# Optimization experiments

Measured on AMD Instinct MI355X. Metric: run time of the kernel, lower is better.

The kernel has to match this reference:

```python
import jax, jax.numpy as jnp
import numpy as np

B, S, HID = 1, 2048, 2048
NH, NKV, D = 16, 8, 128
N_REP = NH // NKV
EPS = 1e-6
ROPE_THETA = 10000.0
N_VISION = 512  # first 512 tokens are vision, rest text


def rms_norm(x, w):
    # RMSNorm over last dim (head_dim), Qwen3 style per-head norm
    var = jnp.mean(x * x, axis=-1, keepdims=True)
    return x * jax.lax.rsqrt(var + EPS) * w


def rotate_half(x):
    half = x.shape[-1] // 2
    return jnp.concatenate([-x[..., half:], x[..., :half]], axis=-1)


def setup_inputs() -> dict:
    key = jax.random.key(0)
    ks = jax.random.split(key, 8)
    std = 0.02
    hidden_states = jax.random.normal(ks[0], (B, S, HID), jnp.float32)
    wq = jax.random.normal(ks[1], (HID, NH * D), jnp.float32) * std
    wk = jax.random.normal(ks[2], (HID, NKV * D), jnp.float32) * std
    wv = jax.random.normal(ks[3], (HID, NKV * D), jnp.float32) * std
    wo = jax.random.normal(ks[4], (NH * D, HID), jnp.float32) * std
    q_norm_w = jnp.ones((D,), jnp.float32)
    k_norm_w = jnp.ones((D,), jnp.float32)
    # RoPE tables: [1, S, D]
    pos = jnp.arange(S, dtype=jnp.float32)
    inv_freq = 1.0 / (ROPE_THETA ** (jnp.arange(0, D, 2, dtype=jnp.float32) / D))
    freqs = pos[:, None] * inv_freq[None, :]            # [S, D/2]
    emb = jnp.concatenate([freqs, freqs], axis=-1)       # [S, D]
    cos = jnp.cos(emb)[None]
    sin = jnp.sin(emb)[None]
    # additive causal mask [1,1,S,S]: 0 on/below diagonal, -1e9 above
    causal = jnp.tril(jnp.ones((S, S), jnp.bool_))
    attention_mask = jnp.where(causal, 0.0, -1e9).astype(jnp.float32)[None, None]
    # vision/text token masks [B, S]
    idx = jnp.arange(S)
    vision_mask = (idx < N_VISION)[None].astype(jnp.bool_)
    text_mask = jnp.logical_not(vision_mask)
    return {
        'hidden_states': hidden_states, 'wq': wq, 'wk': wk, 'wv': wv, 'wo': wo,
        'q_norm_w': q_norm_w, 'k_norm_w': k_norm_w, 'cos': cos, 'sin': sin,
        'attention_mask': attention_mask, 'vision_mask': vision_mask, 'text_mask': text_mask,
    }


def reference(hidden_states, wq, wk, wv, wo, q_norm_w, k_norm_w, cos, sin,
              attention_mask, vision_mask, text_mask):
    b, s, _ = hidden_states.shape
    # projections + per-head RMSNorm (q/k) -> [B, H, S, D]
    q = rms_norm((hidden_states @ wq).reshape(b, s, NH, D), q_norm_w).transpose(0, 2, 1, 3)
    k = rms_norm((hidden_states @ wk).reshape(b, s, NKV, D), k_norm_w).transpose(0, 2, 1, 3)
    v = (hidden_states @ wv).reshape(b, s, NKV, D).transpose(0, 2, 1, 3)
    # RoPE
    c = cos[:, None]  # [B,1,S,D]
    sn = sin[:, None]
    q = q * c + rotate_half(q) * sn
    k = k * c + rotate_half(k) * sn
    # GQA repeat_kv
    k = jnp.repeat(k, N_REP, axis=1)
    v = jnp.repeat(v, N_REP, axis=1)
    scaling = D ** -0.5
    scores = jnp.einsum('bhqd,bhkd->bhqk', q, k) * scaling + attention_mask
    attn = jax.nn.softmax(scores.astype(jnp.float32), axis=-1)  # [B,H,S,S]
    attn_out = jnp.einsum('bhqk,bhkd->bhqd', attn, v)
    attn_out = attn_out.transpose(0, 2, 1, 3).reshape(b, s, NH * D)
    out = attn_out @ wo  # [B,S,HID]
    # cross head scores (original runs this under no_grad on an identical eager pass)
    attn_ng = jax.lax.stop_gradient(attn)
    vm = vision_mask.astype(jnp.float32)  # [B,S]
    tm = text_mask.astype(jnp.float32)
    nv = vm.sum(-1)  # [B]
    nt = tm.sum(-1)
    v2t = jnp.einsum('bhqk,bq,bk->bh', attn_ng, vm, tm) / jnp.maximum(nv, 1.0)[:, None]
    t2v = jnp.einsum('bhqk,bq,bk->bh', attn_ng, tm, vm) / jnp.maximum(nt, 1.0)[:, None]
    valid = ((nv > 0) & (nt > 0)).astype(jnp.float32)  # [B]
    cross_scores = jnp.sum((v2t + t2v) * valid[:, None], axis=0) / jnp.maximum(valid.sum(), 1.0)
    return out, cross_scores
```

## Files before the change

### kernel.cpp

```cpp
#include <hip/hip_runtime.h>
#include <hip/hip_bf16.h>
#include <stdint.h>

typedef unsigned short u16;
typedef unsigned int u32;
typedef short s16x8 __attribute__((ext_vector_type(8)));
typedef float f32x4 __attribute__((ext_vector_type(4)));

#define S_LEN 2048
#define SCALE 0.088388347648318447f
#define NEG_BIG (-1.0e9f)

__device__ __forceinline__ u16 f2bf(float f) {
  unsigned u = __builtin_bit_cast(unsigned, f);
  u += 0x7fffu + ((u >> 16) & 1u);
  return (u16)(u >> 16);
}
__device__ __forceinline__ float bf2f(u16 h) {
  unsigned u = ((unsigned)h) << 16;
  return __builtin_bit_cast(float, u);
}
__device__ __forceinline__ void gload16(const void* g, void* l) {
  __builtin_amdgcn_global_load_lds((const __attribute__((address_space(1))) void*)g,
                                   (__attribute__((address_space(3))) void*)l, 16, 0, 0);
}

__device__ __forceinline__ void do_transpose(const float* __restrict__ in, u16* __restrict__ out,
                                             int R, int C, int rel, int tilesx) {
  __shared__ float tile[32][33];
  int bx = (rel % tilesx) * 32, by = (rel / tilesx) * 32;
  int tx = threadIdx.x & 31, ty = threadIdx.x >> 5;
#pragma unroll
  for (int i = 0; i < 4; i++)
    tile[ty + i * 8][tx] = in[(size_t)(by + ty + i * 8) * C + bx + tx];
  __syncthreads();
#pragma unroll
  for (int i = 0; i < 4; i++)
    out[(size_t)(bx + ty + i * 8) * R + by + tx] = f2bf(tile[tx][ty + i * 8]);
}

__global__ __launch_bounds__(256) void prep_k(const float* __restrict__ hs, u16* __restrict__ hsb,
                                              const float* __restrict__ wq, const float* __restrict__ wk,
                                              const float* __restrict__ wv, const float* __restrict__ wo,
                                              u16* __restrict__ wqkvT, u16* __restrict__ woT) {
  int bid = blockIdx.x;
  if (bid < 4096) {
    int i = bid * 256 + threadIdx.x;
    float4 v = ((const float4*)hs)[i];
    ushort4 o;
    o.x = f2bf(v.x); o.y = f2bf(v.y); o.z = f2bf(v.z); o.w = f2bf(v.w);
    ((ushort4*)hsb)[i] = o;
  } else if (bid < 8192) {
    do_transpose(wq, wqkvT, 2048, 2048, bid - 4096, 64);
  } else if (bid < 10240) {
    do_transpose(wk, wqkvT + (size_t)2048 * 2048, 2048, 1024, bid - 8192, 32);
  } else if (bid < 12288) {
    do_transpose(wv, wqkvT + (size_t)3072 * 2048, 2048, 1024, bid - 10240, 32);
  } else {
    do_transpose(wo, woT, 2048, 2048, bid - 12288, 64);
  }
}

template <int F32OUT>
__global__ __launch_bounds__(256, 2) void gemm_bt_k(const u16* __restrict__ A, const u16* __restrict__ BT,
                                                    void* __restrict__ Cout, int N, int K) {
  __shared__ u16 lA[2][128 * 64];
  __shared__ u16 lB[2][128 * 64];
  int tid = threadIdx.x;
  int w = tid >> 6, l = tid & 63, r = l & 15, g = l >> 4;
  int tn = blockIdx.x, tm = blockIdx.y;
  int wm = w >> 1, wn = w & 1;
  f32x4 zf = {0.f, 0.f, 0.f, 0.f};
  f32x4 acc[4][4];
#pragma unroll
  for (int mi = 0; mi < 4; mi++)
#pragma unroll
    for (int ni = 0; ni < 4; ni++) acc[mi][ni] = zf;
  int nkt = K >> 6;

  int srow = tid >> 3;
  int soff = (tid & 7) * 16;
  auto stage = [&](int bi, int kt) {
#pragma unroll
    for (int i = 0; i < 4; i++) {
      int row = i * 32 + srow;
      int sb = soff ^ ((row & 7) << 4);
      int L = (i * 256 + tid) * 16;
      gload16(A + (size_t)(tm * 128 + row) * K + kt * 64 + (sb >> 1), (char*)(&lA[bi][0]) + L);
      gload16(BT + (size_t)(tn * 128 + row) * K + kt * 64 + (sb >> 1), (char*)(&lB[bi][0]) + L);
    }
  };
  auto compute = [&](int bi) {
    const char* AB = (const char*)&lA[bi][0];
    const char* BB = (const char*)&lB[bi][0];
#pragma unroll
    for (int kk = 0; kk < 2; kk++) {
      s16x8 af[4], bfr[4];
#pragma unroll
      for (int mi = 0; mi < 4; mi++) {
        int row = wm * 64 + mi * 16 + r;
        af[mi] = *(const s16x8*)(AB + ((row * 128 + kk * 64 + g * 16) ^ ((r & 7) << 4)));
      }
#pragma unroll
      for (int ni = 0; ni < 4; ni++) {
        int row = wn * 64 + ni * 16 + r;
        bfr[ni] = *(const s16x8*)(BB + ((row * 128 + kk * 64 + g * 16) ^ ((r & 7) << 4)));
      }
#pragma unroll
      for (int mi = 0; mi < 4; mi++)
#pragma unroll
        for (int ni = 0; ni < 4; ni++)
          acc[mi][ni] = __builtin_amdgcn_mfma_f32_16x16x32_bf16(af[mi], bfr[ni], acc[mi][ni], 0, 0, 0);
    }
  };

  stage(0, 0);
  __syncthreads();
  int cur = 0;
  for (int kt = 0; kt + 1 < nkt; ++kt) {
    stage(cur ^ 1, kt + 1);
    compute(cur);
    __syncthreads();
    cur ^= 1;
  }
  compute(cur);

#pragma unroll
  for (int mi = 0; mi < 4; mi++) {
#pragma unroll
    for (int ni = 0; ni < 4; ni++) {
#pragma unroll
      for (int j = 0; j < 4; j++) {
        int row = tm * 128 + wm * 64 + mi * 16 + g * 4 + j;
        int col = tn * 128 + wn * 64 + ni * 16 + r;
        if (F32OUT)
          ((float*)Cout)[(size_t)row * N + col] = acc[mi][ni][j];
        else
          ((u16*)Cout)[(size_t)row * N + col] = f2bf(acc[mi][ni][j]);
      }
    }
  }
}

__global__ __launch_bounds__(256) void post_k(const u16* __restrict__ qkv, const float* __restrict__ qw,
                                              const float* __restrict__ kw, const float* __restrict__ cosT,
                                              const float* __restrict__ sinT, u16* __restrict__ Qb,
                                              u16* __restrict__ Kb, u16* __restrict__ Vt,
                                              float* __restrict__ cross) {
  int bid = blockIdx.x;
  int tid = threadIdx.x;
  if (bid == 0 && tid < 16) cross[tid] = 0.f;
  if (bid < 16384) {
    int gw = bid * 4 + (tid >> 6);
    int l = tid & 63;
    int s = gw >> 5, slot = gw & 31;
    if (slot >= 24) return;
    const float* nw;
    const u16* src;
    u16* dst;
    if (slot < 16) {
      src = qkv + (size_t)s * 4096 + slot * 128;
      nw = qw;
      dst = Qb + ((size_t)slot * S_LEN + s) * 128;
    } else {
      int hk = slot - 16;
      src = qkv + (size_t)s * 4096 + 2048 + hk * 128;
      nw = kw;
      dst = Kb + ((size_t)hk * S_LEN + s) * 128;
    }
    ushort2 xv = ((const ushort2*)src)[l];
    float x0 = bf2f(xv.x), x1 = bf2f(xv.y);
    float ss = x0 * x0 + x1 * x1;
#pragma unroll
    for (int off = 1; off < 64; off <<= 1) ss += __shfl_xor(ss, off);
    float inv = rsqrtf(ss * (1.0f / 128.0f) + 1e-6f);
    int d0 = l * 2;
    float xn0 = x0 * inv * nw[d0], xn1 = x1 * inv * nw[d0 + 1];
    float p0 = __shfl_xor(xn0, 32), p1 = __shfl_xor(xn1, 32);
    float c0 = cosT[s * 128 + d0], c1 = cosT[s * 128 + d0 + 1];
    float sn0 = sinT[s * 128 + d0], sn1 = sinT[s * 128 + d0 + 1];
    float sg = (l < 32) ? -1.0f : 1.0f;
    ushort2 o;
    o.x = f2bf(xn0 * c0 + sg * p0 * sn0);
    o.y = f2bf(xn1 * c1 + sg * p1 * sn1);
    ((ushort2*)dst)[l] = o;
  } else {
    __shared__ u16 t[64][66];
    int rel = bid - 16384;
    int c0 = (rel & 15) * 64, s0 = (rel >> 4) * 64;
    int tx = tid & 63, ty = tid >> 6;
#pragma unroll
    for (int i = 0; i < 16; i++)
      t[ty + i * 4][tx] = qkv[(size_t)(s0 + ty + i * 4) * 4096 + 3072 + c0 + tx];
    __syncthreads();
#pragma unroll
    for (int i = 0; i < 16; i++)
      Vt[(size_t)(c0 + ty + i * 4) * 2048 + s0 + tx] = t[tx][ty + i * 4];
  }
}

__global__ __launch_bounds__(256, 2) void attn_k(const u16* __restrict__ Qb, const u16* __restrict__ Kb,
                                                 const u16* __restrict__ Vt, u16* __restrict__ AO,
                                                 float* __restrict__ cross) {
  __shared__ u16 Kl[2][64 * 128];
  __shared__ u16 Vl[2][128 * 64];
  __shared__ u16 Pl[4][16 * 64];
  int tid = threadIdx.x;
  int w = tid >> 6, l = tid & 63, r = l & 15, g = l >> 4;
  int bid = blockIdx.x;
  int u = bid & 255, rep = bid >> 8;
  int h = u & 15, a = u >> 4;
  int qb = rep ? (31 - a) : a;
  int hk = h >> 1;
  char* PlB = (char*)(&Pl[w][0]);

  int skrow = tid >> 4;
  int skoff = (tid & 15) * 16;
  int svrow = tid >> 3;
  int svoff = (tid & 7) * 16;
  auto stage = [&](int bi, int kb) {
#pragma unroll
    for (int i = 0; i < 4; i++) {
      int k = i * 16 + skrow;
      int sb = skoff ^ ((k & 7) << 4);
      gload16(Kb + (((size_t)hk * S_LEN + kb * 64 + k) << 7) + (sb >> 1),
              (char*)(&Kl[bi][0]) + (i * 256 + tid) * 16);
    }
#pragma unroll
    for (int i = 0; i < 4; i++) {
      int d = i * 32 + svrow;
      int sb = svoff ^ ((d & 7) << 4);
      gload16(Vt + (((size_t)hk * 128 + d) << 11) + kb * 64 + (sb >> 1),
              (char*)(&Vl[bi][0]) + (i * 256 + tid) * 16);
    }
  };

  int qrow = qb * 64 + w * 16 + r;
  s16x8 qf[4];
#pragma unroll
  for (int kc = 0; kc < 4; kc++)
    qf[kc] = *(const s16x8*)&Qb[((size_t)h * S_LEN + qrow) * 128 + kc * 32 + g * 8];
  f32x4 zf = {0.f, 0.f, 0.f, 0.f};
  f32x4 o_[8];
#pragma unroll
  for (int dt = 0; dt < 8; dt++) o_[dt] = zf;
  float m_ = -3e38f, l_ = 0.f, vs_ = 0.f;

  stage(0, 0);
  __syncthreads();
  int buf = 0;
  for (int kb = 0; kb <= qb; ++kb) {
    if (kb < qb) stage(buf ^ 1, kb + 1);
    const char* KB = (const char*)&Kl[buf][0];
    const char* VB = (const char*)&Vl[buf][0];
    f32x4 sa[4];
    __builtin_amdgcn_s_setprio(1);
#pragma unroll
    for (int ct = 0; ct < 4; ct++) {
      sa[ct] = zf;
#pragma unroll
      for (int kc = 0; kc < 4; kc++) {
        int kbyte = (((ct * 16 + r) * 256) + kc * 64 + g * 16) ^ ((r & 7) << 4);
        sa[ct] = __builtin_amdgcn_mfma_f32_16x16x32_bf16(*(const s16x8*)(KB + kbyte), qf[kc], sa[ct], 0, 0, 0);
      }
    }
    __builtin_amdgcn_s_setprio(0);
    float sv[4][4];
    float rmax = -3e38f;
    if (kb == qb) {
      int kb0 = kb * 64 + g * 4;
#pragma unroll
      for (int ct = 0; ct < 4; ct++)
#pragma unroll
        for (int j = 0; j < 4; j++) {
          float x = sa[ct][j] * SCALE + ((kb0 + ct * 16 + j) > qrow ? NEG_BIG : 0.f);
          sv[ct][j] = x;
          rmax = fmaxf(rmax, x);
        }
    } else {
#pragma unroll
      for (int ct = 0; ct < 4; ct++)
#pragma unroll
        for (int j = 0; j < 4; j++) {
          float x = sa[ct][j] * SCALE;
          sv[ct][j] = x;
          rmax = fmaxf(rmax, x);
        }
    }
    rmax = fmaxf(rmax, __shfl_xor(rmax, 16));
    rmax = fmaxf(rmax, __shfl_xor(rmax, 32));
    if (__any(rmax > m_ + 8.f)) {
      float mn = fmaxf(m_, rmax);
      float sc = __expf(m_ - mn);
      m_ = mn;
      l_ *= sc;
      vs_ *= sc;
      float scb[4];
#pragma unroll
      for (int j = 0; j < 4; j++) scb[j] = __shfl(sc, g * 4 + j);
#pragma unroll
      for (int dt = 0; dt < 8; dt++)
#pragma unroll
        for (int j = 0; j < 4; j++) o_[dt][j] *= scb[j];
    }
    float t = 0.f;
#pragma unroll
    for (int ct = 0; ct < 4; ct++)
#pragma unroll
      for (int j = 0; j < 4; j++) {
        float p = __expf(sv[ct][j] - m_);
        sv[ct][j] = p;
        t += p;
      }
    t += __shfl_xor(t, 16);
    t += __shfl_xor(t, 32);
    l_ += t;
    if (kb < 8) vs_ += t;
#pragma unroll
    for (int ct = 0; ct < 4; ct++) {
      uint2 pw;
      pw.x = (u32)f2bf(sv[ct][0]) | ((u32)f2bf(sv[ct][1]) << 16);
      pw.y = (u32)f2bf(sv[ct][2]) | ((u32)f2bf(sv[ct][3]) << 16);
      *(uint2*)(PlB + ((r * 128 + ct * 32 + g * 8) ^ ((r & 7) << 4))) = pw;
    }
    s16x8 pf[2];
#pragma unroll
    for (int kc = 0; kc < 2; kc++)
      pf[kc] = *(const s16x8*)(PlB + ((r * 128 + kc * 64 + g * 16) ^ ((r & 7) << 4)));
    __builtin_amdgcn_s_setprio(1);
#pragma unroll
    for (int dt = 0; dt < 8; dt++)
#pragma unroll
      for (int kc = 0; kc < 2; kc++) {
        int vbyte = (((dt * 16 + r) * 128) + kc * 64 + g * 16) ^ ((r & 7) << 4);
        o_[dt] = __builtin_amdgcn_mfma_f32_16x16x32_bf16(pf[kc], *(const s16x8*)(VB + vbyte), o_[dt], 0, 0, 0);
      }
    __builtin_amdgcn_s_setprio(0);
    __syncthreads();
    buf ^= 1;
  }
  float lb[4];
#pragma unroll
  for (int j = 0; j < 4; j++) lb[j] = 1.0f / __shfl(l_, g * 4 + j);
#pragma unroll
  for (int dt = 0; dt < 8; dt++)
#pragma unroll
    for (int j = 0; j < 4; j++) {
      int row = qb * 64 + w * 16 + g * 4 + j;
      int col = h * 128 + dt * 16 + r;
      AO[(size_t)row * 2048 + col] = f2bf(o_[dt][j] * lb[j]);
    }
  if (qb >= 8) {
    float acc = vs_ / l_;
#pragma unroll
    for (int off = 1; off < 64; off <<= 1) acc += __shfl_xor(acc, off);
    if (l == 0) atomicAdd(&cross[h], acc * (1.0f / (4.0f * 1536.0f)));
  }
}

extern "C" void kernel_launch(void* const* d_in, const int* in_sizes, int n_in,
                              void* d_out, int out_size, void* d_ws, size_t ws_size,
                              hipStream_t stream) {
  const float* hs = (const float*)d_in[0];
  const float* wq = (const float*)d_in[1];
  const float* wk = (const float*)d_in[2];
  const float* wv = (const float*)d_in[3];
  const float* wo = (const float*)d_in[4];
  const float* qw = (const float*)d_in[5];
  const float* kw = (const float*)d_in[6];
  const float* cosT = (const float*)d_in[7];
  const float* sinT = (const float*)d_in[8];
  float* out = (float*)d_out;
  float* cross = out + (size_t)2048 * 2048;
  char* ws = (char*)d_ws;
  u16* hsb = (u16*)ws;
  u16* wqkvT = (u16*)(ws + (8u << 20));
  u16* woT = (u16*)(ws + (24u << 20));
  u16* qkvb = (u16*)(ws + (32u << 20));
  u16* AO = hsb;
  u16* Qb = wqkvT;
  u16* Kb = (u16*)(ws + (16u << 20));
  u16* Vt = (u16*)(ws + (20u << 20));

  prep_k<<<16384, 256, 0, stream>>>(hs, hsb, wq, wk, wv, wo, wqkvT, woT);
  gemm_bt_k<0><<<dim3(32, 16), 256, 0, stream>>>(hsb, wqkvT, qkvb, 4096, 2048);
  post_k<<<16896, 256, 0, stream>>>(qkvb, qw, kw, cosT, sinT, Qb, Kb, Vt, cross);
  attn_k<<<512, 256, 0, stream>>>(Qb, Kb, Vt, AO, cross);
  gemm_bt_k<1><<<dim3(16, 16), 256, 0, stream>>>(AO, woT, out, 2048, 2048);
}
```

Baseline: 282.6 us.

## Overlap loads with compute via vmcnt waits, fold softmax scale into Q, 256-row QKV GEMM

The GEMM and attention loops now issue the next tile's global-to-LDS loads, wait with explicit vmcnt counts, and use raw s_barrier instead of __syncthreads, so the prefetch of the next buffer stays in flight while the current one is computed. The QKV projection GEMM moves to 256-row tiles with 512 threads to raise operand reuse. The softmax scale is folded into Q during post-processing, removing a multiply per score, and attention block indices are reordered to interleave short and long causal rows. The hand-written waitcnt values must exactly match the number of loads issued, and rounding scaled Q to bf16 slightly changes numerics.

```diff
diff --git a/kernel.cpp b/kernel.cpp
--- a/kernel.cpp
+++ b/kernel.cpp
@@ -10,6 +10,8 @@
 #define S_LEN 2048
 #define SCALE 0.088388347648318447f
 #define NEG_BIG (-1.0e9f)
+#define WAITV(N) asm volatile("s_waitcnt vmcnt(" #N ")" ::: "memory")
+#define FENCE() asm volatile("" ::: "memory")
 
 __device__ __forceinline__ u16 f2bf(float f) {
   unsigned u = __builtin_bit_cast(unsigned, f);
@@ -61,10 +63,14 @@
   }
 }
 
-template <int F32OUT>
-__global__ __launch_bounds__(256, 2) void gemm_bt_k(const u16* __restrict__ A, const u16* __restrict__ BT,
-                                                    void* __restrict__ Cout, int N, int K) {
-  __shared__ u16 lA[2][128 * 64];
+template <int BM, int F32OUT>
+__global__ __launch_bounds__(BM == 256 ? 512 : 256, 2) void gemm2_k(const u16* __restrict__ A,
+                                                                    const u16* __restrict__ BT,
+                                                                    void* __restrict__ Cout, int N, int K) {
+  constexpr int NT = (BM == 256) ? 512 : 256;
+  constexpr int ALOADS = BM * 8 / NT;
+  constexpr int BLOADS = 128 * 8 / NT;
+  __shared__ u16 lA[2][BM * 64];
   __shared__ u16 lB[2][128 * 64];
   int tid = threadIdx.x;
   int w = tid >> 6, l = tid & 63, r = l & 15, g = l >> 4;
@@ -78,16 +84,20 @@
     for (int ni = 0; ni < 4; ni++) acc[mi][ni] = zf;
   int nkt = K >> 6;
 
-  int srow = tid >> 3;
-  int soff = (tid & 7) * 16;
   auto stage = [&](int bi, int kt) {
 #pragma unroll
-    for (int i = 0; i < 4; i++) {
-      int row = i * 32 + srow;
-      int sb = soff ^ ((row & 7) << 4);
-      int L = (i * 256 + tid) * 16;
-      gload16(A + (size_t)(tm * 128 + row) * K + kt * 64 + (sb >> 1), (char*)(&lA[bi][0]) + L);
-      gload16(BT + (size_t)(tn * 128 + row) * K + kt * 64 + (sb >> 1), (char*)(&lB[bi][0]) + L);
+    for (int i = 0; i < ALOADS; i++) {
+      int c = i * NT + tid;
+      int row = c >> 3;
+      int sb = ((c & 7) * 16) ^ ((row & 7) << 4);
+      gload16(A + (size_t)(tm * BM + row) * K + kt * 64 + (sb >> 1), (char*)(&lA[bi][0]) + c * 16);
+    }
+#pragma unroll
+    for (int i = 0; i < BLOADS; i++) {
+      int c = i * NT + tid;
+      int row = c >> 3;
+      int sb = ((c & 7) * 16) ^ ((row & 7) << 4);
+      gload16(BT + (size_t)(tn * 128 + row) * K + kt * 64 + (sb >> 1), (char*)(&lB[bi][0]) + c * 16);
     }
   };
   auto compute = [&](int bi) {
@@ -115,15 +125,23 @@
   };
 
   stage(0, 0);
-  __syncthreads();
   int cur = 0;
-  for (int kt = 0; kt + 1 < nkt; ++kt) {
-    stage(cur ^ 1, kt + 1);
+  for (int kt = 0; kt < nkt; ++kt) {
+    if (kt + 1 < nkt) {
+      stage(cur ^ 1, kt + 1);
+      if (BM == 256) WAITV(6); else WAITV(8);
+    } else {
+      WAITV(0);
+    }
+    FENCE();
+    __builtin_amdgcn_s_barrier();
+    FENCE();
     compute(cur);
-    __syncthreads();
+    FENCE();
+    __builtin_amdgcn_s_barrier();
+    FENCE();
     cur ^= 1;
   }
-  compute(cur);
 
 #pragma unroll
   for (int mi = 0; mi < 4; mi++) {
@@ -131,7 +149,7 @@
     for (int ni = 0; ni < 4; ni++) {
 #pragma unroll
       for (int j = 0; j < 4; j++) {
-        int row = tm * 128 + wm * 64 + mi * 16 + g * 4 + j;
+        int row = tm * BM + wm * 64 + mi * 16 + g * 4 + j;
         int col = tn * 128 + wn * 64 + ni * 16 + r;
         if (F32OUT)
           ((float*)Cout)[(size_t)row * N + col] = acc[mi][ni][j];
@@ -158,15 +176,18 @@
     const float* nw;
     const u16* src;
     u16* dst;
+    float qs;
     if (slot < 16) {
       src = qkv + (size_t)s * 4096 + slot * 128;
       nw = qw;
       dst = Qb + ((size_t)slot * S_LEN + s) * 128;
+      qs = SCALE;
     } else {
       int hk = slot - 16;
       src = qkv + (size_t)s * 4096 + 2048 + hk * 128;
       nw = kw;
       dst = Kb + ((size_t)hk * S_LEN + s) * 128;
+      qs = 1.0f;
     }
     ushort2 xv = ((const ushort2*)src)[l];
     float x0 = bf2f(xv.x), x1 = bf2f(xv.y);
@@ -181,8 +202,8 @@
     float sn0 = sinT[s * 128 + d0], sn1 = sinT[s * 128 + d0 + 1];
     float sg = (l < 32) ? -1.0f : 1.0f;
     ushort2 o;
-    o.x = f2bf(xn0 * c0 + sg * p0 * sn0);
-    o.y = f2bf(xn1 * c1 + sg * p1 * sn1);
+    o.x = f2bf((xn0 * c0 + sg * p0 * sn0) * qs);
+    o.y = f2bf((xn1 * c1 + sg * p1 * sn1) * qs);
     ((ushort2*)dst)[l] = o;
   } else {
     __shared__ u16 t[64][66];
@@ -208,9 +229,10 @@
   int tid = threadIdx.x;
   int w = tid >> 6, l = tid & 63, r = l & 15, g = l >> 4;
   int bid = blockIdx.x;
-  int u = bid & 255, rep = bid >> 8;
-  int h = u & 15, a = u >> 4;
-  int qb = rep ? (31 - a) : a;
+  int sel = (bid >> 4) & 1;
+  int idx = (bid & 15) | ((bid >> 5) << 4);
+  int h = idx & 15, a = idx >> 4;
+  int qb = sel ? (31 - a) : a;
   int hk = h >> 1;
   char* PlB = (char*)(&Pl[w][0]);
 
@@ -247,10 +269,17 @@
   float m_ = -3e38f, l_ = 0.f, vs_ = 0.f;
 
   stage(0, 0);
-  __syncthreads();
   int buf = 0;
   for (int kb = 0; kb <= qb; ++kb) {
-    if (kb < qb) stage(buf ^ 1, kb + 1);
+    if (kb < qb) {
+      stage(buf ^ 1, kb + 1);
+      WAITV(8);
+    } else {
+      WAITV(0);
+    }
+    FENCE();
+    __builtin_amdgcn_s_barrier();
+    FENCE();
     const char* KB = (const char*)&Kl[buf][0];
     const char* VB = (const char*)&Vl[buf][0];
     f32x4 sa[4];
@@ -273,7 +302,7 @@
       for (int ct = 0; ct < 4; ct++)
 #pragma unroll
         for (int j = 0; j < 4; j++) {
-          float x = sa[ct][j] * SCALE + ((kb0 + ct * 16 + j) > qrow ? NEG_BIG : 0.f);
+          float x = sa[ct][j] + ((kb0 + ct * 16 + j) > qrow ? NEG_BIG : 0.f);
           sv[ct][j] = x;
           rmax = fmaxf(rmax, x);
         }
@@ -282,7 +311,7 @@
       for (int ct = 0; ct < 4; ct++)
 #pragma unroll
         for (int j = 0; j < 4; j++) {
-          float x = sa[ct][j] * SCALE;
+          float x = sa[ct][j];
           sv[ct][j] = x;
           rmax = fmaxf(rmax, x);
         }
@@ -336,7 +365,9 @@
         o_[dt] = __builtin_amdgcn_mfma_f32_16x16x32_bf16(pf[kc], *(const s16x8*)(VB + vbyte), o_[dt], 0, 0, 0);
       }
     __builtin_amdgcn_s_setprio(0);
-    __syncthreads();
+    FENCE();
+    __builtin_amdgcn_s_barrier();
+    FENCE();
     buf ^= 1;
   }
   float lb[4];
@@ -383,8 +414,8 @@
   u16* Vt = (u16*)(ws + (20u << 20));
 
   prep_k<<<16384, 256, 0, stream>>>(hs, hsb, wq, wk, wv, wo, wqkvT, woT);
-  gemm_bt_k<0><<<dim3(32, 16), 256, 0, stream>>>(hsb, wqkvT, qkvb, 4096, 2048);
+  gemm2_k<256, 0><<<dim3(32, 8), 512, 0, stream>>>(hsb, wqkvT, qkvb, 4096, 2048);
   post_k<<<16896, 256, 0, stream>>>(qkvb, qw, kw, cosT, sinT, Qb, Kb, Vt, cross);
   attn_k<<<512, 256, 0, stream>>>(Qb, Kb, Vt, AO, cross);
-  gemm_bt_k<1><<<dim3(16, 16), 256, 0, stream>>>(AO, woT, out, 2048, 2048);
-}
+  gemm2_k<128, 1><<<dim3(16, 16), 256, 0, stream>>>(AO, woT, out, 2048, 2048);
+}
```

Result: slower. 289.2 us (+2.3%).
